# Optimization experiments

Hardware: AMD Instinct MI355X
Metric: run time of the kernel (lower is better)

## Reference

```python
import jax, jax.numpy as jnp
import numpy as np

N, L, DV, EF = 64, 128, 16, 4
D, H, FF, LC, K, MS = 256, 8, 1024, 3, 6, 16
DK = D // H
NEG = -1e9


def _ln(x, g, b):
    m = x.mean(-1, keepdims=True)
    v = ((x - m) ** 2).mean(-1, keepdims=True)
    return (x - m) / jnp.sqrt(v + 1e-5) * g + b


def setup_inputs() -> dict:
    key = jax.random.key(0)
    ks = jax.random.split(key, 20)
    s = 0.05
    rn = lambda k, sh: jax.random.normal(k, sh, jnp.float32) * s
    return {
        "vehicles": jax.random.normal(ks[0], (N, L, DV), jnp.float32),
        "fleet_edges": jax.random.uniform(ks[1], (N, L, L, EF), jnp.float32),
        "Wproj": rn(ks[2], (DV, D)), "bproj": jnp.zeros((D,), jnp.float32),
        "Wq": rn(ks[3], (LC, D, D)), "Wk": rn(ks[4], (LC, D, D)), "Wv": rn(ks[5], (LC, D, D)),
        "mix1_w": rn(ks[6], (LC, H, 2, MS)), "mix1_b": jnp.zeros((LC, H, MS), jnp.float32),
        "mix2_w": rn(ks[7], (LC, H, MS)), "mix2_b": jnp.zeros((LC, H), jnp.float32),
        "Wo": rn(ks[8], (LC, D, D)), "bo": jnp.zeros((LC, D), jnp.float32),
        "n1_g": jnp.ones((LC, D), jnp.float32), "n1_b": jnp.zeros((LC, D), jnp.float32),
        "ff1_w": rn(ks[9], (LC, D, FF)), "ff1_b": jnp.zeros((LC, FF), jnp.float32),
        "ff2_w": rn(ks[10], (LC, FF, D)), "ff2_b": jnp.zeros((LC, D), jnp.float32),
        "n2_g": jnp.ones((LC, D), jnp.float32), "n2_b": jnp.zeros((LC, D), jnp.float32),
    }


def _forward(vehicles, fleet_edges, Wproj, bproj, Wq, Wk, Wv, mix1_w, mix1_b,
             mix2_w, mix2_b, Wo, bo, n1_g, n1_b, ff1_w, ff1_b, ff2_w, ff2_b, n2_g, n2_b):
    h = vehicles @ Wproj + bproj                      # (N, L, D)
    dist = fleet_edges[..., 0]                        # (N, L, L)
    cost = dist
    # kNN mask: keep K smallest distances per row; mask==True -> blocked
    _, knn_idx = jax.lax.top_k(-dist, K)              # (N, L, K)
    nbr = jnp.any(jax.nn.one_hot(knn_idx, L, dtype=bool), axis=2)  # (N, L, L)
    mask = ~nbr
    row_fully_masked = mask.all(-1)                   # (N, L)
    inv_sqrt_dk = 1.0 / np.sqrt(DK).astype(np.float32)
    for i in range(LC):
        q = (h @ Wq[i]).reshape(N, L, H, DK).transpose(0, 2, 1, 3)
        k_ = (h @ Wk[i]).reshape(N, L, H, DK).transpose(0, 2, 1, 3)
        v = (h @ Wv[i]).reshape(N, L, H, DK).transpose(0, 2, 1, 3)
        dot = jnp.einsum('nhrd,nhcd->nhrc', q, k_) * inv_sqrt_dk      # (N,H,L,L)
        cost_b = jnp.broadcast_to(cost[:, None], (N, H, L, L))
        two = jnp.stack([dot, cost_b], axis=-1)                        # (N,H,L,L,2)
        ms1 = jax.nn.relu(jnp.einsum('nhrct,htm->nhrcm', two, mix1_w[i])
                          + mix1_b[i][None, :, None, None, :])         # (N,H,L,L,MS)
        score = jnp.einsum('nhrcm,hm->nhrc', ms1, mix2_w[i]) \
                + mix2_b[i][None, :, None, None]                       # (N,H,L,L)
        score = jnp.where(mask[:, None], NEG, score)
        w = jax.nn.softmax(score, axis=-1)
        att = jnp.einsum('nhrc,nhcd->nhrd', w, v)
        att = att.transpose(0, 2, 1, 3).reshape(N, L, D) @ Wo[i] + bo[i]
        h1 = _ln(h + att, n1_g[i], n1_b[i])
        ff = jax.nn.relu(h1 @ ff1_w[i] + ff1_b[i]) @ ff2_w[i] + ff2_b[i]
        h = _ln(h1 + ff, n2_g[i], n2_b[i])
        # original does h_out[mask] = 0; with kNN k>0 every row keeps k entries,
        # so only fully-masked rows would be zeroed (a no-op here, kept for fidelity)
        h = jnp.where(row_fully_masked[..., None], 0.0, h)
    return h


def reference(vehicles, fleet_edges, Wproj, bproj, Wq, Wk, Wv, mix1_w, mix1_b,
              mix2_w, mix2_b, Wo, bo, n1_g, n1_b, ff1_w, ff1_b, ff2_w, ff2_b, n2_g, n2_b):
    return _forward(vehicles, fleet_edges, Wproj, bproj, Wq, Wk, Wv, mix1_w, mix1_b,
                    mix2_w, mix2_b, Wo, bo, n1_g, n1_b, ff1_w, ff1_b, ff2_w, ff2_b, n2_g, n2_b)
```

## Files before the change

### kernel.cpp

```cpp
#include <hip/hip_runtime.h>
#include <math.h>

#define NB 64
#define LL 128
#define DV 16
#define DD 256
#define HH 8
#define DK 32
#define FF 1024
#define LC 3
#define KNN 6
#define MS 16
#define WLS 786432

typedef __attribute__((ext_vector_type(8))) short s16x8;
typedef __attribute__((ext_vector_type(4))) float f32x4;

static __device__ inline unsigned short f2b(float x) {
    union { float f; unsigned int u; } v; v.f = x;
    unsigned int r = (v.u + 0x7FFFu + ((v.u >> 16) & 1u)) >> 16;
    return (unsigned short)r;
}

static __device__ __forceinline__ void glds16(const void* g, void* l) {
    __builtin_amdgcn_global_load_lds(
        (const __attribute__((address_space(1))) void*)g,
        (__attribute__((address_space(3))) void*)l, 16, 0, 0);
}

__global__ __launch_bounds__(256)
void uber_pre(const float* __restrict__ veh, const float* __restrict__ Wp,
              const float* __restrict__ bp, float* __restrict__ h,
              unsigned short* __restrict__ hb,
              const float* __restrict__ edges, unsigned long long* __restrict__ idx8,
              const float* __restrict__ Wq, const float* __restrict__ Wk,
              const float* __restrict__ Wv, const float* __restrict__ Wo,
              const float* __restrict__ f1, const float* __restrict__ f2,
              unsigned short* __restrict__ Wt) {
    int bx = blockIdx.x;
    if (bx < 2048) {
        int m = bx * 4 + (threadIdx.x >> 6);
        int l = threadIdx.x & 63;
        int c0 = l * 4;
        const float4* w4 = reinterpret_cast<const float4*>(Wp);
        float4 a = *reinterpret_cast<const float4*>(bp + c0);
        const float* vr = veh + (size_t)m * DV;
#pragma unroll
        for (int t = 0; t < DV; ++t) {
            float vt = vr[t];
            float4 wv = w4[t * 64 + l];
            a.x += vt * wv.x; a.y += vt * wv.y; a.z += vt * wv.z; a.w += vt * wv.w;
        }
        *reinterpret_cast<float4*>(h + (size_t)m * DD + c0) = a;
        ushort4 u; u.x = f2b(a.x); u.y = f2b(a.y); u.z = f2b(a.z); u.w = f2b(a.w);
        *reinterpret_cast<ushort4*>(hb + (size_t)m * DD + c0) = u;
        return;
    }
    if (bx < 4096) {
        int row = (bx - 2048) * 4 + (threadIdx.x >> 6);
        int lane = threadIdx.x & 63;
        const float* dr = edges + (size_t)row * LL * 4;
        float v0 = dr[lane * 4], v1 = dr[(lane + 64) * 4];
        int i0 = lane, i1 = lane + 64;
        unsigned long long packed = 0;
#pragma unroll
        for (int k = 0; k < KNN; ++k) {
            float v; int i;
            if (v1 < v0) { v = v1; i = i1; } else { v = v0; i = i0; }
#pragma unroll
            for (int o = 1; o < 64; o <<= 1) {
                float ov = __shfl_xor(v, o);
                int oi = __shfl_xor(i, o);
                if (ov < v || (ov == v && oi < i)) { v = ov; i = oi; }
            }
            packed |= (unsigned long long)i << (k * 8);
            if (i == i0) v0 = 3.4e38f;
            if (i == i1) v1 = 3.4e38f;
        }
        if (lane == 0) idx8[row] = packed;
        return;
    }
    {
        int t = bx - 4096;
        int ll = t / 768, r = t % 768;
        int w, tile, K, N;
        if (r < 256)      { w = r >> 6; tile = r & 63;  K = DD; N = DD; }
        else if (r < 512) { w = 4; tile = r - 256;      K = DD; N = FF; }
        else              { w = 5; tile = r - 512;      K = FF; N = DD; }
        const float* src = (w == 0) ? Wq : (w == 1) ? Wk : (w == 2) ? Wv :
                           (w == 3) ? Wo : (w == 4) ? f1 : f2;
        src += (size_t)ll * K * N;
        long off = (w == 4) ? 262144L : (w == 5) ? 524288L : (long)w * 65536L;
        unsigned short* dst = Wt + (size_t)ll * WLS + off;
        int ntx = N >> 5;
        int n0 = (tile % ntx) * 32, k0 = (tile / ntx) * 32;
        int tx = threadIdx.x & 31, ty = threadIdx.x >> 5;
        __shared__ float T[32][33];
#pragma unroll
        for (int rr = 0; rr < 4; ++rr)
            T[ty + rr * 8][tx] = src[(size_t)(k0 + ty + rr * 8) * N + n0 + tx];
        __syncthreads();
#pragma unroll
        for (int rr = 0; rr < 4; ++rr)
            dst[(size_t)(n0 + ty + rr * 8) * K + k0 + tx] = f2b(T[tx][ty + rr * 8]);
    }
}

template <int BM, int BN, int WR, int WC, int MODE>
__global__ __launch_bounds__(256)
void gg(const unsigned short* __restrict__ A, const unsigned short* __restrict__ Bt,
        const float* __restrict__ bias, unsigned short* __restrict__ Cb,
        float* __restrict__ Oq, float* __restrict__ Ok, float* __restrict__ Ov,
        int K, int N) {
    constexpr int MI = BM / (WR * 16);
    constexpr int NJ = BN / (WC * 16);
    __shared__ unsigned short As[BM * 32];
    __shared__ unsigned short Bs[BN * 32];
    int tid = threadIdx.x;
    int w = tid >> 6, l = tid & 63;
    int lr = l & 15, lg = l >> 4;
    int wr = w % WR, wc = w / WR;
    int m0 = blockIdx.y * BM, n0 = blockIdx.x * BN;
    int row = tid >> 2, seg = tid & 3;

    f32x4 acc[MI][NJ];
#pragma unroll
    for (int i = 0; i < MI; ++i)
#pragma unroll
        for (int j = 0; j < NJ; ++j) acc[i][j] = (f32x4)(0.f);

    for (int k0 = 0; k0 < K; k0 += 32) {
        __syncthreads();
#pragma unroll
        for (int r = 0; r < BM / 64; ++r)
            glds16(A + (size_t)(m0 + r * 64 + row) * K + k0 + seg * 8,
                   As + r * 2048 + w * 512);
#pragma unroll
        for (int r = 0; r < BN / 64; ++r)
            glds16(Bt + (size_t)(n0 + r * 64 + row) * K + k0 + seg * 8,
                   Bs + r * 2048 + w * 512);
        __syncthreads();
        s16x8 af[MI], bf[NJ];
#pragma unroll
        for (int i = 0; i < MI; ++i)
            af[i] = *reinterpret_cast<const s16x8*>(
                As + (wr * MI * 16 + i * 16 + lr) * 32 + lg * 8);
#pragma unroll
        for (int j = 0; j < NJ; ++j)
            bf[j] = *reinterpret_cast<const s16x8*>(
                Bs + (wc * NJ * 16 + j * 16 + lr) * 32 + lg * 8);
#pragma unroll
        for (int i = 0; i < MI; ++i)
#pragma unroll
            for (int j = 0; j < NJ; ++j)
                acc[i][j] = __builtin_amdgcn_mfma_f32_16x16x32_bf16(af[i], bf[j], acc[i][j], 0, 0, 0);
    }

    if constexpr (MODE == 2) {
        int s = n0 >> 8;
        float* dst = (s == 0) ? Oq : (s == 1) ? Ok : Ov;
#pragma unroll
        for (int i = 0; i < MI; ++i)
#pragma unroll
            for (int j = 0; j < NJ; ++j) {
                int cc = (n0 & 255) + wc * NJ * 16 + j * 16 + lr;
                int hh = cc >> 5, dk = cc & 31;
                int grow = m0 + wr * MI * 16 + i * 16 + lg * 4;
                int nn = grow >> 7, rl = grow & 127;
                size_t ho = ((size_t)(nn * HH + hh) * LL + rl) * DK + dk;
#pragma unroll
                for (int q = 0; q < 4; ++q)
                    dst[ho + (size_t)q * DK] = acc[i][j][q];
            }
    } else {
#pragma unroll
        for (int i = 0; i < MI; ++i)
#pragma unroll
            for (int j = 0; j < NJ; ++j) {
                int col = n0 + wc * NJ * 16 + j * 16 + lr;
                float bc = bias[col];
#pragma unroll
                for (int q = 0; q < 4; ++q) {
                    int r = m0 + wr * MI * 16 + i * 16 + lg * 4 + q;
                    float v = fmaxf(acc[i][j][q] + bc, 0.f);
                    Cb[(size_t)r * N + col] = f2b(v);
                }
            }
    }
}

template <int KK, bool ATT>
__global__ __launch_bounds__(256)
void gg_ln(const unsigned short* __restrict__ A, const unsigned short* __restrict__ Bt,
           const float* __restrict__ qh, const float* __restrict__ kh,
           const float* __restrict__ vh, const float* __restrict__ edges,
           const unsigned long long* __restrict__ idx8,
           const float* __restrict__ m1w, const float* __restrict__ m1b,
           const float* __restrict__ m2w, const float* __restrict__ m2b,
           const float* __restrict__ bias, const float* __restrict__ res,
           const float* __restrict__ g, const float* __restrict__ be,
           float* __restrict__ out, unsigned short* __restrict__ outb) {
    constexpr int ASTRIDE = ATT ? 264 : 32;
    __shared__ unsigned short As[16 * ASTRIDE];
    __shared__ unsigned short Bs[256 * 32];
    __shared__ float Red[16][4];
    int tid = threadIdx.x;
    int w = tid >> 6, l = tid & 63;
    int lr = l & 15, lg = l >> 4;
    int m0 = blockIdx.x * 16;

    if constexpr (ATT) {
        int task = tid >> 1, sub = tid & 1;
        int rl = task & 15, hh = task >> 4;
        int n = m0 >> 7, r = (m0 & 127) + rl;
        int bh = n * HH + hh;
        const float scale = 0.17677669529663687f;
        const float* w0g = m1w + (hh * 2 + 0) * MS;
        const float* w1g = m1w + (hh * 2 + 1) * MS;
        const float* b1g = m1b + hh * MS;
        const float* w2g = m2w + hh * MS;
        float b2v = m2b[hh];

        const float4* qr = reinterpret_cast<const float4*>(
            qh + ((size_t)bh * LL + r) * DK) + sub * 4;
        float4 q[4];
#pragma unroll
        for (int j = 0; j < 4; ++j) q[j] = qr[j];

        unsigned long long pk = idx8[(size_t)n * LL + r];
        const float* kbase = kh + (size_t)bh * LL * DK;
        const float* vbase = vh + (size_t)bh * LL * DK;
        const float* erow = edges + (size_t)(n * LL + r) * LL * 4;

        int col[KNN];
#pragma unroll
        for (int k = 0; k < KNN; ++k) col[k] = (int)((pk >> (k * 8)) & 0xFF);

        float e[KNN];
        float mx = -3.4e38f;
#pragma unroll
        for (int k = 0; k < KNN; ++k) {
            const float4* kr = reinterpret_cast<const float4*>(
                kbase + (size_t)col[k] * DK) + sub * 4;
            float d = 0.f;
#pragma unroll
            for (int j = 0; j < 4; ++j) {
                float4 kv = kr[j];
                d += q[j].x * kv.x + q[j].y * kv.y + q[j].z * kv.z + q[j].w * kv.w;
            }
            d += __shfl_xor(d, 1);
            d *= scale;
            float cst = erow[col[k] * 4];
            float s = b2v;
#pragma unroll
            for (int m = 0; m < MS; ++m)
                s += fmaxf(d * w0g[m] + cst * w1g[m] + b1g[m], 0.f) * w2g[m];
            e[k] = s;
            mx = fmaxf(mx, s);
        }
        float sum = 0.f;
#pragma unroll
        for (int k = 0; k < KNN; ++k) { e[k] = __expf(e[k] - mx); sum += e[k]; }
        float inv = 1.f / sum;

        float4 att[4];
#pragma unroll
        for (int j = 0; j < 4; ++j) att[j] = make_float4(0.f, 0.f, 0.f, 0.f);
#pragma unroll
        for (int k = 0; k < KNN; ++k) {
            float wgt = e[k] * inv;
            const float4* vr = reinterpret_cast<const float4*>(
                vbase + (size_t)col[k] * DK) + sub * 4;
#pragma unroll
            for (int j = 0; j < 4; ++j) {
                float4 vv = vr[j];
                att[j].x += wgt * vv.x; att[j].y += wgt * vv.y;
                att[j].z += wgt * vv.z; att[j].w += wgt * vv.w;
            }
        }
        unsigned short* arow = As + rl * ASTRIDE + hh * DK + sub * 16;
#pragma unroll
        for (int j = 0; j < 4; ++j) {
            ushort4 u;
            u.x = f2b(att[j].x); u.y = f2b(att[j].y);
            u.z = f2b(att[j].z); u.w = f2b(att[j].w);
            *reinterpret_cast<ushort4*>(arow + j * 4) = u;
        }
    }

    f32x4 acc[4];
#pragma unroll
    for (int j = 0; j < 4; ++j) acc[j] = (f32x4)(0.f);

    for (int k0 = 0; k0 < KK; k0 += 32) {
        __syncthreads();
        if constexpr (!ATT) {
            if (w == 0)
                glds16(A + (size_t)(m0 + (l >> 2)) * KK + k0 + (l & 3) * 8, As);
        }
#pragma unroll
        for (int i = 0; i < 4; ++i) {
            int idx = w * 4 + i;
            glds16(Bt + (size_t)(idx * 16 + (l >> 2)) * KK + k0 + (l & 3) * 8,
                   Bs + idx * 512);
        }
        __syncthreads();
        s16x8 af;
        if constexpr (ATT)
            af = *reinterpret_cast<const s16x8*>(As + lr * ASTRIDE + k0 + lg * 8);
        else
            af = *reinterpret_cast<const s16x8*>(As + lr * ASTRIDE + lg * 8);
#pragma unroll
        for (int j = 0; j < 4; ++j) {
            s16x8 bf = *reinterpret_cast<const s16x8*>(
                Bs + (w * 64 + j * 16 + lr) * 32 + lg * 8);
            acc[j] = __builtin_amdgcn_mfma_f32_16x16x32_bf16(af, bf, acc[j], 0, 0, 0);
        }
    }

    float rsum[4] = {0.f, 0.f, 0.f, 0.f};
#pragma unroll
    for (int j = 0; j < 4; ++j) {
        int col = w * 64 + j * 16 + lr;
        float bc = bias[col];
#pragma unroll
        for (int q = 0; q < 4; ++q) {
            float x = acc[j][q] + bc + res[(size_t)(m0 + lg * 4 + q) * DD + col];
            acc[j][q] = x;
            rsum[q] += x;
        }
    }
#pragma unroll
    for (int q = 0; q < 4; ++q)
#pragma unroll
        for (int o = 1; o < 16; o <<= 1) rsum[q] += __shfl_xor(rsum[q], o);
    __syncthreads();
    if (lr == 0)
#pragma unroll
        for (int q = 0; q < 4; ++q) Red[lg * 4 + q][w] = rsum[q];
    __syncthreads();
    float mean[4];
#pragma unroll
    for (int q = 0; q < 4; ++q) {
        int row = lg * 4 + q;
        mean[q] = (Red[row][0] + Red[row][1] + Red[row][2] + Red[row][3]) * (1.0f / 256.0f);
    }
    float ssum[4] = {0.f, 0.f, 0.f, 0.f};
#pragma unroll
    for (int j = 0; j < 4; ++j)
#pragma unroll
        for (int q = 0; q < 4; ++q) {
            float d = acc[j][q] - mean[q];
            ssum[q] += d * d;
        }
#pragma unroll
    for (int q = 0; q < 4; ++q)
#pragma unroll
        for (int o = 1; o < 16; o <<= 1) ssum[q] += __shfl_xor(ssum[q], o);
    __syncthreads();
    if (lr == 0)
#pragma unroll
        for (int q = 0; q < 4; ++q) Red[lg * 4 + q][w] = ssum[q];
    __syncthreads();
    float rstd[4];
#pragma unroll
    for (int q = 0; q < 4; ++q) {
        int row = lg * 4 + q;
        float var = (Red[row][0] + Red[row][1] + Red[row][2] + Red[row][3]) * (1.0f / 256.0f);
        rstd[q] = 1.0f / sqrtf(var + 1e-5f);
    }
#pragma unroll
    for (int j = 0; j < 4; ++j) {
        int col = w * 64 + j * 16 + lr;
        float gc = g[col], bc2 = be[col];
#pragma unroll
        for (int q = 0; q < 4; ++q) {
            size_t off = (size_t)(m0 + lg * 4 + q) * DD + col;
            float v = (acc[j][q] - mean[q]) * rstd[q] * gc + bc2;
            out[off] = v;
            outb[off] = f2b(v);
        }
    }
}

extern "C" void kernel_launch(void* const* d_in, const int* in_sizes, int n_in,
                              void* d_out, int out_size, void* d_ws, size_t ws_size,
                              hipStream_t stream) {
    const float* vehicles = (const float*)d_in[0];
    const float* fleet    = (const float*)d_in[1];
    const float* Wproj    = (const float*)d_in[2];
    const float* bproj    = (const float*)d_in[3];
    const float* Wq       = (const float*)d_in[4];
    const float* Wk       = (const float*)d_in[5];
    const float* Wv       = (const float*)d_in[6];
    const float* m1w      = (const float*)d_in[7];
    const float* m1b      = (const float*)d_in[8];
    const float* m2w      = (const float*)d_in[9];
    const float* m2b      = (const float*)d_in[10];
    const float* Wo       = (const float*)d_in[11];
    const float* bo       = (const float*)d_in[12];
    const float* n1_g     = (const float*)d_in[13];
    const float* n1_b     = (const float*)d_in[14];
    const float* ff1_w    = (const float*)d_in[15];
    const float* ff1_b    = (const float*)d_in[16];
    const float* ff2_w    = (const float*)d_in[17];
    const float* ff2_b    = (const float*)d_in[18];
    const float* n2_g     = (const float*)d_in[19];
    const float* n2_b     = (const float*)d_in[20];

    const size_t MROWS = (size_t)NB * LL;
    const size_t HSZ   = MROWS * DD;

    float* ws = (float*)d_ws;
    float* h   = ws;
    float* qh  = h + HSZ;
    float* kh  = qh + HSZ;
    float* vh  = kh + HSZ;
    unsigned short* hb    = (unsigned short*)(vh + HSZ);
    unsigned short* ffmid = hb + HSZ;
    unsigned short* Wt    = ffmid + MROWS * FF;
    unsigned long long* idx8 = (unsigned long long*)(Wt + 3 * WLS);

    uber_pre<<<6400, 256, 0, stream>>>(vehicles, Wproj, bproj, h, hb,
                                       fleet, idx8,
                                       Wq, Wk, Wv, Wo, ff1_w, ff2_w, Wt);

    dim3 gqkv(12, 128);
    dim3 gff1(8, 128);

    for (int i = 0; i < LC; ++i) {
        const unsigned short* wt = Wt + (size_t)i * WLS;

        gg<64, 64, 2, 2, 2><<<gqkv, 256, 0, stream>>>(
            hb, wt, nullptr, nullptr, qh, kh, vh, DD, 768);

        gg_ln<256, true><<<512, 256, 0, stream>>>(
            nullptr, wt + 196608,
            qh, kh, vh, fleet, idx8,
            m1w + (size_t)i * HH * 2 * MS, m1b + (size_t)i * HH * MS,
            m2w + (size_t)i * HH * MS,     m2b + (size_t)i * HH,
            bo + (size_t)i * DD,
            h, n1_g + (size_t)i * DD, n1_b + (size_t)i * DD, h, hb);

        gg<64, 128, 2, 2, 1><<<gff1, 256, 0, stream>>>(
            hb, wt + 262144, ff1_b + (size_t)i * FF, ffmid,
            nullptr, nullptr, nullptr, DD, FF);

        float* dst = (i == LC - 1) ? (float*)d_out : h;
        gg_ln<1024, false><<<512, 256, 0, stream>>>(
            ffmid, wt + 524288,
            nullptr, nullptr, nullptr, nullptr, nullptr,
            nullptr, nullptr, nullptr, nullptr,
            ff2_b + (size_t)i * DD,
            h, n2_g + (size_t)i * DD, n2_b + (size_t)i * DD, dst, hb);
    }
}
```

Baseline: 241.1 us.

## Double-buffer LDS tiles in the GEMM and GEMM+LayerNorm kernels

Both MFMA GEMM kernels now keep two LDS buffers for the A and B k-tiles. The next k-slice is issued into the spare buffer right after the barrier, before the current slice is read, so global-to-LDS loads can overlap the MFMA work and the loop needs one barrier per step instead of two. In the attention-fused variant, the full attention row buffer is moved into its own array and only B is double-buffered. The cost is doubled LDS use for the staging tiles, which may lower occupancy.

```diff
diff --git a/kernel.cpp b/kernel.cpp
--- a/kernel.cpp
+++ b/kernel.cpp
@@ -114,8 +114,8 @@
         int K, int N) {
     constexpr int MI = BM / (WR * 16);
     constexpr int NJ = BN / (WC * 16);
-    __shared__ unsigned short As[BM * 32];
-    __shared__ unsigned short Bs[BN * 32];
+    __shared__ unsigned short As[2][BM * 32];
+    __shared__ unsigned short Bs[2][BN * 32];
     int tid = threadIdx.x;
     int w = tid >> 6, l = tid & 63;
     int lr = l & 15, lg = l >> 4;
@@ -123,32 +123,38 @@
     int m0 = blockIdx.y * BM, n0 = blockIdx.x * BN;
     int row = tid >> 2, seg = tid & 3;
 
-    f32x4 acc[MI][NJ];
-#pragma unroll
-    for (int i = 0; i < MI; ++i)
-#pragma unroll
-        for (int j = 0; j < NJ; ++j) acc[i][j] = (f32x4)(0.f);
-
-    for (int k0 = 0; k0 < K; k0 += 32) {
-        __syncthreads();
+    auto STAGE = [&](int buf, int k0) {
 #pragma unroll
         for (int r = 0; r < BM / 64; ++r)
             glds16(A + (size_t)(m0 + r * 64 + row) * K + k0 + seg * 8,
-                   As + r * 2048 + w * 512);
+                   As[buf] + r * 2048 + w * 512);
 #pragma unroll
         for (int r = 0; r < BN / 64; ++r)
             glds16(Bt + (size_t)(n0 + r * 64 + row) * K + k0 + seg * 8,
-                   Bs + r * 2048 + w * 512);
+                   Bs[buf] + r * 2048 + w * 512);
+    };
+
+    f32x4 acc[MI][NJ];
+#pragma unroll
+    for (int i = 0; i < MI; ++i)
+#pragma unroll
+        for (int j = 0; j < NJ; ++j) acc[i][j] = (f32x4)(0.f);
+
+    STAGE(0, 0);
+    int nsteps = K >> 5;
+    for (int step = 0; step < nsteps; ++step) {
+        int cur = step & 1;
         __syncthreads();
+        if (step + 1 < nsteps) STAGE(cur ^ 1, (step + 1) * 32);
         s16x8 af[MI], bf[NJ];
 #pragma unroll
         for (int i = 0; i < MI; ++i)
             af[i] = *reinterpret_cast<const s16x8*>(
-                As + (wr * MI * 16 + i * 16 + lr) * 32 + lg * 8);
+                As[cur] + (wr * MI * 16 + i * 16 + lr) * 32 + lg * 8);
 #pragma unroll
         for (int j = 0; j < NJ; ++j)
             bf[j] = *reinterpret_cast<const s16x8*>(
-                Bs + (wc * NJ * 16 + j * 16 + lr) * 32 + lg * 8);
+                Bs[cur] + (wc * NJ * 16 + j * 16 + lr) * 32 + lg * 8);
 #pragma unroll
         for (int i = 0; i < MI; ++i)
 #pragma unroll
@@ -200,9 +206,9 @@
            const float* __restrict__ bias, const float* __restrict__ res,
            const float* __restrict__ g, const float* __restrict__ be,
            float* __restrict__ out, unsigned short* __restrict__ outb) {
-    constexpr int ASTRIDE = ATT ? 264 : 32;
-    __shared__ unsigned short As[16 * ASTRIDE];
-    __shared__ unsigned short Bs[256 * 32];
+    __shared__ unsigned short Afull[ATT ? 16 * 264 : 1];
+    __shared__ unsigned short As[ATT ? 1 : 2][16 * 32];
+    __shared__ unsigned short Bs[2][256 * 32];
     __shared__ float Red[16][4];
     int tid = threadIdx.x;
     int w = tid >> 6, l = tid & 63;
@@ -278,7 +284,7 @@
                 att[j].z += wgt * vv.z; att[j].w += wgt * vv.w;
             }
         }
-        unsigned short* arow = As + rl * ASTRIDE + hh * DK + sub * 16;
+        unsigned short* arow = Afull + rl * 264 + hh * DK + sub * 16;
 #pragma unroll
         for (int j = 0; j < 4; ++j) {
             ushort4 u;
@@ -288,32 +294,38 @@
         }
     }
 
-    f32x4 acc[4];
-#pragma unroll
-    for (int j = 0; j < 4; ++j) acc[j] = (f32x4)(0.f);
-
-    for (int k0 = 0; k0 < KK; k0 += 32) {
-        __syncthreads();
+    auto STAGE = [&](int buf, int k0) {
         if constexpr (!ATT) {
             if (w == 0)
-                glds16(A + (size_t)(m0 + (l >> 2)) * KK + k0 + (l & 3) * 8, As);
+                glds16(A + (size_t)(m0 + (l >> 2)) * KK + k0 + (l & 3) * 8, As[buf]);
         }
 #pragma unroll
         for (int i = 0; i < 4; ++i) {
             int idx = w * 4 + i;
             glds16(Bt + (size_t)(idx * 16 + (l >> 2)) * KK + k0 + (l & 3) * 8,
-                   Bs + idx * 512);
-        }
+                   Bs[buf] + idx * 512);
+        }
+    };
+
+    f32x4 acc[4];
+#pragma unroll
+    for (int j = 0; j < 4; ++j) acc[j] = (f32x4)(0.f);
+
+    STAGE(0, 0);
+    constexpr int NSTEPS = KK >> 5;
+    for (int step = 0; step < NSTEPS; ++step) {
+        int cur = step & 1;
         __syncthreads();
+        if (step + 1 < NSTEPS) STAGE(cur ^ 1, (step + 1) * 32);
         s16x8 af;
         if constexpr (ATT)
-            af = *reinterpret_cast<const s16x8*>(As + lr * ASTRIDE + k0 + lg * 8);
+            af = *reinterpret_cast<const s16x8*>(Afull + lr * 264 + step * 32 + lg * 8);
         else
-            af = *reinterpret_cast<const s16x8*>(As + lr * ASTRIDE + lg * 8);
+            af = *reinterpret_cast<const s16x8*>(As[cur] + lr * 32 + lg * 8);
 #pragma unroll
         for (int j = 0; j < 4; ++j) {
             s16x8 bf = *reinterpret_cast<const s16x8*>(
-                Bs + (w * 64 + j * 16 + lr) * 32 + lg * 8);
+                Bs[cur] + (w * 64 + j * 16 + lr) * 32 + lg * 8);
             acc[j] = __builtin_amdgcn_mfma_f32_16x16x32_bf16(af, bf, acc[j], 0, 0, 0);
         }
     }
```

Result: faster. 227.7 us (-5.6%).
